# Optimization experiments

Hardware: AMD Instinct MI355X
Metric: run time of the kernel (lower is better)

## Reference

```python
import jax, jax.numpy as jnp
import numpy as np

B, C, H, W = 8, 256, 64, 64
HEADS, H_SP, W_SP = 8, 64, 4  # idx=0: H_sp=resolution[0], W_sp=split_size
D = C // HEADS
SCALE = D ** -0.5
HH, WW = H // H_SP, W // W_SP  # 1, 16 (no padding needed)


def setup_inputs() -> dict:
    key = jax.random.key(0)
    k1, k2, k3 = jax.random.split(key, 3)
    temp = jax.random.normal(k1, (B, 3, C, H, W), dtype=jnp.float32)
    get_v_weight = jax.random.normal(k2, (C, 1, 3, 3), dtype=jnp.float32) * 0.1
    get_v_bias = jax.random.normal(k3, (C,), dtype=jnp.float32) * 0.1
    return {"temp": temp, "get_v_weight": get_v_weight, "get_v_bias": get_v_bias}


def _im2win_shuffle(x):
    # x: (B, C, H, W); H split as (H_SP, HH) with H_SP OUTER (shuffled windows)
    x = x.reshape(B, HEADS, D, H_SP, HH, W_SP, WW)
    x = x.transpose(0, 4, 6, 1, 3, 5, 2)  # b hh ww h H_sp W_sp d
    return x.reshape(B * HH * WW, HEADS, H_SP * W_SP, D)


def reference(temp, get_v_weight, get_v_bias):
    # H, W are multiples of H_SP, W_SP -> pad is zero (faithful to F.pad path)
    q, k, v = temp[:, 0], temp[:, 1], temp[:, 2]
    qw = _im2win_shuffle(q) * SCALE
    kw = _im2win_shuffle(k)
    vw = _im2win_shuffle(v)

    # LePE: depthwise 3x3 conv applied per shuffled window
    vimg = v.reshape(B, C, H_SP, HH, W_SP, WW).transpose(0, 3, 5, 1, 2, 4)
    vimg = vimg.reshape(B * HH * WW, C, H_SP, W_SP)
    lepe = jax.lax.conv_general_dilated(
        vimg, get_v_weight, (1, 1), ((1, 1), (1, 1)),
        dimension_numbers=("NCHW", "OIHW", "NCHW"), feature_group_count=C,
    ) + get_v_bias[None, :, None, None]
    lepe = lepe.reshape(B * HH * WW, HEADS, D, H_SP * W_SP).transpose(0, 1, 3, 2)

    attn = jax.nn.softmax(jnp.einsum("whqd,whkd->whqk", qw, kw), axis=-1)
    x = jnp.einsum("whqk,whkd->whqd", attn, vw) + lepe  # (nW, h, S, d)

    # windows2img_shuffle -> (B, C, H, W), then raw .view to (B, H, W, C)
    x = x.reshape(B, HH, WW, HEADS, H_SP, W_SP, D)
    x = x.transpose(0, 3, 6, 4, 1, 5, 2).reshape(B, C, H, W)
    x = x.reshape(B, H, W, C)  # raw memory view, matches torch .view
    return x.reshape(B, H * W, C)
```

## Files before the change

### kernel.cpp

```cpp
#include <hip/hip_runtime.h>


typedef __attribute__((ext_vector_type(8))) short bf16x8;
typedef __attribute__((ext_vector_type(4))) float floatx4;
typedef unsigned short ushort_t;
typedef unsigned int uint_t;

constexpr float QSCALE = 0.25503486f;

__device__ __forceinline__ ushort_t f2bf(float f) {
    union { float f; uint_t u; } v; v.f = f;
    uint_t r = v.u + 0x7fffu + ((v.u >> 16) & 1u);
    return (ushort_t)(r >> 16);
}
__device__ __forceinline__ float bf2f(ushort_t h) {
    union { uint_t u; float f; } v; v.u = ((uint_t)h) << 16;
    return v.f;
}

constexpr int KSP = 10240;
constexpr int VTB = 4 * KSP;
constexpr int VTP = 8448;
constexpr int OPITCH = 33;
constexpr int OBP = 256 * OPITCH;

__global__ __attribute__((amdgpu_waves_per_eu(4, 4))) __launch_bounds__(1024)
void fused_kernel(const float* __restrict__ temp, const float* __restrict__ wgt,
                  const float* __restrict__ bias, float* __restrict__ out)
{
    const int bid = blockIdx.x;
    const int hd = bid & 7, b = (bid >> 3) & 7, wwg = bid >> 6;

    __shared__ __align__(16) ushort_t SM[74752];

    const int u = threadIdx.x;
    const int g = u >> 6, p = g >> 2, wv = g & 3;
    const int ln = u & 63;
    const int lm = ln & 15, q4 = ln >> 4, l7 = ln & 7, b8 = (ln >> 3) & 1;

    const float4* Tq = (const float4*)temp + (((size_t)(b * 3) * 256 + hd * 32) * 1024 + wwg);
    const float4* Tk = Tq + (size_t)256 * 1024;
    const float4* Tv = Tk + (size_t)256 * 1024;

    union F4 { float4 v; float a[4]; };

    #pragma unroll
    for (int i = 0; i < 4; i++) {
        const int flat = i * 1024 + u;
        const int t = flat & 255, d2 = flat >> 8;
        const int d = d2 * 2;
        F4 v0, v1;
        v0.v = Tq[(size_t)d * 1024 + t * 4];
        v1.v = Tq[(size_t)(d + 1) * 1024 + t * 4];
        #pragma unroll
        for (int pp = 0; pp < 4; pp++) {
            const uint_t pk = (uint_t)f2bf(v0.a[pp] * QSCALE)
                            | ((uint_t)f2bf(v1.a[pp] * QSCALE) << 16);
            *(uint_t*)&SM[pp * KSP + t * 40 + d] = pk;
        }
    }
    __syncthreads();

    bf16x8 qa[4];
    #pragma unroll
    for (int T = 0; T < 4; T++) {
        const int Tg = wv * 4 + T;
        qa[T] = *(const bf16x8*)&SM[p * KSP + (Tg * 16 + lm) * 40 + q4 * 8];
    }
    __syncthreads();

    #pragma unroll
    for (int i = 0; i < 4; i++) {
        const int flat = i * 1024 + u;
        const int t = flat & 255, d2 = flat >> 8;
        const int d = d2 * 2;
        F4 v0, v1;
        v0.v = Tk[(size_t)d * 1024 + t * 4];
        v1.v = Tk[(size_t)(d + 1) * 1024 + t * 4];
        #pragma unroll
        for (int pp = 0; pp < 4; pp++) {
            const uint_t pk = (uint_t)f2bf(v0.a[pp]) | ((uint_t)f2bf(v1.a[pp]) << 16);
            *(uint_t*)&SM[pp * KSP + t * 40 + d] = pk;
        }
    }
    #pragma unroll
    for (int i = 0; i < 8; i++) {
        const int flat = i * 1024 + u;
        const int t = flat & 255, d = flat >> 8;
        F4 va;
        va.v = Tv[(size_t)d * 1024 + t * 4];
        #pragma unroll
        for (int pp = 0; pp < 4; pp++)
            SM[VTB + pp * VTP + d * 264 + t] = f2bf(va.a[pp]);
    }
    __syncthreads();

    const int pK = p * KSP;
    const int pV = VTB + p * VTP;
    const int pa_w0 = pK + (wv * 64 + b8 * 16 + q4 * 4) * 40 + 32 + l7;
    const int pa_w1 = pK + (wv * 64 + (2 + b8) * 16 + q4 * 4) * 40 + 32 + l7;
    const int pa_rd = pK + (wv * 64 + ln) * 40 + 32;

    floatx4 acc[4][2];
    float lrow[4][4];
    #pragma unroll
    for (int T = 0; T < 4; T++) {
        acc[T][0] = (floatx4)0.0f; acc[T][1] = (floatx4)0.0f;
        #pragma unroll
        for (int r = 0; r < 4; r++) lrow[T][r] = 0.0f;
    }

    for (int c = 0; c < 8; c++) {
        const bf16x8 kb0 = *(const bf16x8*)&SM[pK + (c * 32 + lm) * 40 + q4 * 8];
        const bf16x8 kb1 = *(const bf16x8*)&SM[pK + (c * 32 + 16 + lm) * 40 + q4 * 8];
        const bf16x8 vb0 = *(const bf16x8*)&SM[pV + lm * 264 + c * 32 + q4 * 8];
        const bf16x8 vb1 = *(const bf16x8*)&SM[pV + (16 + lm) * 264 + c * 32 + q4 * 8];
        #pragma unroll
        for (int T = 0; T < 4; T++) {
            floatx4 s0 = __builtin_amdgcn_mfma_f32_16x16x32_bf16(qa[T], kb0, (floatx4)0.0f, 0, 0, 0);
            floatx4 s1 = __builtin_amdgcn_mfma_f32_16x16x32_bf16(qa[T], kb1, (floatx4)0.0f, 0, 0, 0);
            #pragma unroll
            for (int r = 0; r < 4; r++) {
                const float p0 = exp2f(s0[r]);
                const float p1 = exp2f(s1[r]);
                const ushort_t h0 = f2bf(p0), h1 = f2bf(p1);
                lrow[T][r] += bf2f(h0) + bf2f(h1);
                SM[pa_w0 + r * 40] = h0;
                SM[pa_w1 + r * 40] = h1;
            }
            const bf16x8 pa = *(const bf16x8*)&SM[pa_rd];
            acc[T][0] = __builtin_amdgcn_mfma_f32_16x16x32_bf16(pa, vb0, acc[T][0], 0, 0, 0);
            acc[T][1] = __builtin_amdgcn_mfma_f32_16x16x32_bf16(pa, vb1, acc[T][1], 0, 0, 0);
        }
    }

    float wc[2][9], bs2[2];
    #pragma unroll
    for (int dt = 0; dt < 2; dt++) {
        const int d = dt * 16 + lm;
        #pragma unroll
        for (int k = 0; k < 9; k++) wc[dt][k] = wgt[(hd * 32 + d) * 9 + k];
        bs2[dt] = bias[hd * 32 + d];
    }

    #pragma unroll
    for (int T = 0; T < 4; T++) {
        const int Tg = wv * 4 + T;
        const int hs = Tg * 4 + q4;
        float inv[4];
        #pragma unroll
        for (int r = 0; r < 4; r++) {
            float ls = lrow[T][r];
            ls += __shfl_xor(ls, 1); ls += __shfl_xor(ls, 2);
            ls += __shfl_xor(ls, 4); ls += __shfl_xor(ls, 8);
            inv[r] = 1.0f / ls;
        }
        #pragma unroll
        for (int dt = 0; dt < 2; dt++) {
            const int d = dt * 16 + lm;
            float vv[3][4];
            #pragma unroll
            for (int dy = 0; dy < 3; dy++) {
                const int hh = hs + dy - 1;
                if (hh >= 0 && hh < 64) {
                    #pragma unroll
                    for (int cx = 0; cx < 4; cx++) vv[dy][cx] = bf2f(SM[pV + d * 264 + hh * 4 + cx]);
                } else {
                    #pragma unroll
                    for (int cx = 0; cx < 4; cx++) vv[dy][cx] = 0.0f;
                }
            }
            #pragma unroll
            for (int r = 0; r < 4; r++) {
                float lep = bs2[dt];
                #pragma unroll
                for (int dy = 0; dy < 3; dy++) {
                    #pragma unroll
                    for (int kx = 0; kx < 3; kx++) {
                        const int wsrc = r + kx - 1;
                        if (wsrc >= 0 && wsrc < 4) lep += wc[dt][dy * 3 + kx] * vv[dy][wsrc];
                    }
                }
                acc[T][dt][r] = acc[T][dt][r] * inv[r] + lep;
            }
        }
    }
    __syncthreads();

    float* Ob = (float*)SM;
    #pragma unroll
    for (int T = 0; T < 4; T++) {
        const int Tg = wv * 4 + T;
        #pragma unroll
        for (int dt = 0; dt < 2; dt++) {
            const int d = dt * 16 + lm;
            #pragma unroll
            for (int r = 0; r < 4; r++) {
                const int q = Tg * 16 + q4 * 4 + r;
                Ob[p * OBP + q * OPITCH + d] = acc[T][dt][r];
            }
        }
    }
    __syncthreads();

    float4* out4 = (float4*)out + (((size_t)(b * 256) + hd * 32) * 1024 + wwg);
    #pragma unroll
    for (int i = 0; i < 8; i++) {
        const int flat = i * 1024 + u;
        const int t = flat & 255, d = flat >> 8;
        float4 o;
        o.x = Ob[0 * OBP + t * OPITCH + d];
        o.y = Ob[1 * OBP + t * OPITCH + d];
        o.z = Ob[2 * OBP + t * OPITCH + d];
        o.w = Ob[3 * OBP + t * OPITCH + d];
        out4[(size_t)d * 1024 + t * 4] = o;
    }
}

extern "C" void kernel_launch(void* const* d_in, const int* in_sizes, int n_in,
                              void* d_out, int out_size, void* d_ws, size_t ws_size,
                              hipStream_t stream) {
    const float* temp = (const float*)d_in[0];
    const float* wgt  = (const float*)d_in[1];
    const float* bias = (const float*)d_in[2];
    float* out = (float*)d_out;
    (void)d_ws; (void)ws_size;
    fused_kernel<<<dim3(256), dim3(1024), 0, stream>>>(temp, wgt, bias, out);
}
```

Before: 205.4 us.

## Split work into 512 blocks of two windows and swizzle K/Q LDS columns

Each block now handles 2 windows instead of 4, so the grid doubles to 512 blocks of 512 threads and each block uses half the LDS. Global loads become float2 instead of float4. An XOR swizzle on the Q/K LDS column layout is added to reduce bank conflicts on MFMA operand reads. The aim is more blocks per CU and better latency hiding, at the cost of narrower, less coalesced global accesses.

After: 214.6 us. 4.5% more time.

```diff
diff --git a/kernel.cpp b/kernel.cpp
--- a/kernel.cpp
+++ b/kernel.cpp
@@ -19,87 +19,84 @@
 }
 
 constexpr int KSP = 10240;
-constexpr int VTB = 4 * KSP;
+constexpr int VTB = 2 * KSP;
 constexpr int VTP = 8448;
 constexpr int OPITCH = 33;
 constexpr int OBP = 256 * OPITCH;
 
-__global__ __attribute__((amdgpu_waves_per_eu(4, 4))) __launch_bounds__(1024)
+__global__ __launch_bounds__(512) __attribute__((amdgpu_waves_per_eu(4, 4)))
 void fused_kernel(const float* __restrict__ temp, const float* __restrict__ wgt,
                   const float* __restrict__ bias, float* __restrict__ out)
 {
     const int bid = blockIdx.x;
-    const int hd = bid & 7, b = (bid >> 3) & 7, wwg = bid >> 6;
-
-    __shared__ __align__(16) ushort_t SM[74752];
+    const int hd = bid & 7, b = (bid >> 3) & 7, wg2 = bid >> 6;
+
+    __shared__ __align__(16) ushort_t SM[37376];
 
     const int u = threadIdx.x;
     const int g = u >> 6, p = g >> 2, wv = g & 3;
     const int ln = u & 63;
     const int lm = ln & 15, q4 = ln >> 4, l7 = ln & 7, b8 = (ln >> 3) & 1;
-
-    const float4* Tq = (const float4*)temp + (((size_t)(b * 3) * 256 + hd * 32) * 1024 + wwg);
-    const float4* Tk = Tq + (size_t)256 * 1024;
-    const float4* Tv = Tk + (size_t)256 * 1024;
-
-    union F4 { float4 v; float a[4]; };
-
-    #pragma unroll
-    for (int i = 0; i < 4; i++) {
-        const int flat = i * 1024 + u;
+    const int l8 = lm >> 3;
+
+    const float2* Tq2 = (const float2*)temp + ((size_t)((b * 3 + 0) * 256 + hd * 32)) * 2048 + wg2;
+    const float2* Tk2 = Tq2 + (size_t)256 * 2048;
+    const float2* Tv2 = Tk2 + (size_t)256 * 2048;
+
+    #pragma unroll
+    for (int i = 0; i < 8; i++) {
+        const int flat = i * 512 + u;
         const int t = flat & 255, d2 = flat >> 8;
         const int d = d2 * 2;
-        F4 v0, v1;
-        v0.v = Tq[(size_t)d * 1024 + t * 4];
-        v1.v = Tq[(size_t)(d + 1) * 1024 + t * 4];
-        #pragma unroll
-        for (int pp = 0; pp < 4; pp++) {
-            const uint_t pk = (uint_t)f2bf(v0.a[pp] * QSCALE)
-                            | ((uint_t)f2bf(v1.a[pp] * QSCALE) << 16);
-            *(uint_t*)&SM[pp * KSP + t * 40 + d] = pk;
-        }
-    }
-    __syncthreads();
-
+        const int col = (((d2 >> 2) ^ ((t >> 3) & 3)) << 3) + ((d2 & 3) << 1);
+        const float2 v0 = Tq2[(size_t)d * 2048 + t * 8];
+        const float2 v1 = Tq2[(size_t)(d + 1) * 2048 + t * 8];
+        const uint_t p0 = (uint_t)f2bf(v0.x * QSCALE) | ((uint_t)f2bf(v1.x * QSCALE) << 16);
+        const uint_t p1 = (uint_t)f2bf(v0.y * QSCALE) | ((uint_t)f2bf(v1.y * QSCALE) << 16);
+        *(uint_t*)&SM[t * 40 + col] = p0;
+        *(uint_t*)&SM[KSP + t * 40 + col] = p1;
+    }
+    __syncthreads();
+
+    const int pK = p * KSP;
+    const int pV = VTB + p * VTP;
     bf16x8 qa[4];
     #pragma unroll
     for (int T = 0; T < 4; T++) {
         const int Tg = wv * 4 + T;
-        qa[T] = *(const bf16x8*)&SM[p * KSP + (Tg * 16 + lm) * 40 + q4 * 8];
-    }
-    __syncthreads();
-
-    #pragma unroll
-    for (int i = 0; i < 4; i++) {
-        const int flat = i * 1024 + u;
+        const int s = ((Tg & 1) << 1) + l8;
+        qa[T] = *(const bf16x8*)&SM[pK + (Tg * 16 + lm) * 40 + ((q4 ^ s) << 3)];
+    }
+    __syncthreads();
+
+    #pragma unroll
+    for (int i = 0; i < 8; i++) {
+        const int flat = i * 512 + u;
         const int t = flat & 255, d2 = flat >> 8;
         const int d = d2 * 2;
-        F4 v0, v1;
-        v0.v = Tk[(size_t)d * 1024 + t * 4];
-        v1.v = Tk[(size_t)(d + 1) * 1024 + t * 4];
-        #pragma unroll
-        for (int pp = 0; pp < 4; pp++) {
-            const uint_t pk = (uint_t)f2bf(v0.a[pp]) | ((uint_t)f2bf(v1.a[pp]) << 16);
-            *(uint_t*)&SM[pp * KSP + t * 40 + d] = pk;
-        }
-    }
-    #pragma unroll
-    for (int i = 0; i < 8; i++) {
-        const int flat = i * 1024 + u;
+        const int col = (((d2 >> 2) ^ ((t >> 3) & 3)) << 3) + ((d2 & 3) << 1);
+        const float2 v0 = Tk2[(size_t)d * 2048 + t * 8];
+        const float2 v1 = Tk2[(size_t)(d + 1) * 2048 + t * 8];
+        const uint_t p0 = (uint_t)f2bf(v0.x) | ((uint_t)f2bf(v1.x) << 16);
+        const uint_t p1 = (uint_t)f2bf(v0.y) | ((uint_t)f2bf(v1.y) << 16);
+        *(uint_t*)&SM[t * 40 + col] = p0;
+        *(uint_t*)&SM[KSP + t * 40 + col] = p1;
+    }
+    #pragma unroll
+    for (int i = 0; i < 16; i++) {
+        const int flat = i * 512 + u;
         const int t = flat & 255, d = flat >> 8;
-        F4 va;
-        va.v = Tv[(size_t)d * 1024 + t * 4];
-        #pragma unroll
-        for (int pp = 0; pp < 4; pp++)
-            SM[VTB + pp * VTP + d * 264 + t] = f2bf(va.a[pp]);
-    }
-    __syncthreads();
-
-    const int pK = p * KSP;
-    const int pV = VTB + p * VTP;
+        const float2 va = Tv2[(size_t)d * 2048 + t * 8];
+        SM[VTB + d * 264 + t] = f2bf(va.x);
+        SM[VTB + VTP + d * 264 + t] = f2bf(va.y);
+    }
+    __syncthreads();
+
     const int pa_w0 = pK + (wv * 64 + b8 * 16 + q4 * 4) * 40 + 32 + l7;
     const int pa_w1 = pK + (wv * 64 + (2 + b8) * 16 + q4 * 4) * 40 + 32 + l7;
     const int pa_rd = pK + (wv * 64 + ln) * 40 + 32;
+    const int kcol0 = (q4 ^ l8) << 3;
+    const int kcol1 = (q4 ^ (2 + l8)) << 3;
 
     floatx4 acc[4][2];
     float lrow[4][4];
@@ -111,8 +108,8 @@
     }
 
     for (int c = 0; c < 8; c++) {
-        const bf16x8 kb0 = *(const bf16x8*)&SM[pK + (c * 32 + lm) * 40 + q4 * 8];
-        const bf16x8 kb1 = *(const bf16x8*)&SM[pK + (c * 32 + 16 + lm) * 40 + q4 * 8];
+        const bf16x8 kb0 = *(const bf16x8*)&SM[pK + (c * 32 + lm) * 40 + kcol0];
+        const bf16x8 kb1 = *(const bf16x8*)&SM[pK + (c * 32 + 16 + lm) * 40 + kcol1];
         const bf16x8 vb0 = *(const bf16x8*)&SM[pV + lm * 264 + c * 32 + q4 * 8];
         const bf16x8 vb1 = *(const bf16x8*)&SM[pV + (16 + lm) * 264 + c * 32 + q4 * 8];
         #pragma unroll
@@ -203,17 +200,15 @@
     }
     __syncthreads();
 
-    float4* out4 = (float4*)out + (((size_t)(b * 256) + hd * 32) * 1024 + wwg);
-    #pragma unroll
-    for (int i = 0; i < 8; i++) {
-        const int flat = i * 1024 + u;
+    float2* out2 = (float2*)out + ((size_t)(b * 256 + hd * 32)) * 2048 + wg2;
+    #pragma unroll
+    for (int i = 0; i < 16; i++) {
+        const int flat = i * 512 + u;
         const int t = flat & 255, d = flat >> 8;
-        float4 o;
+        float2 o;
         o.x = Ob[0 * OBP + t * OPITCH + d];
         o.y = Ob[1 * OBP + t * OPITCH + d];
-        o.z = Ob[2 * OBP + t * OPITCH + d];
-        o.w = Ob[3 * OBP + t * OPITCH + d];
-        out4[(size_t)d * 1024 + t * 4] = o;
+        out2[(size_t)d * 2048 + t * 8] = o;
     }
 }
 
@@ -225,5 +220,5 @@
     const float* bias = (const float*)d_in[2];
     float* out = (float*)d_out;
     (void)d_ws; (void)ws_size;
-    fused_kernel<<<dim3(256), dim3(1024), 0, stream>>>(temp, wgt, bias, out);
-}
+    fused_kernel<<<dim3(512), dim3(512), 0, stream>>>(temp, wgt, bias, out);
+}
```
